# Optimization experiments

Hardware: AMD Instinct MI355X
Metric: run time of the kernel (lower is better)

The kernel has to match this reference:

```python
import jax, jax.numpy as jnp
import numpy as np

H = 16
D_MODEL = 1024
D_K = D_MODEL // H


def setup_inputs() -> dict:
    key = jax.random.key(0)
    ks = jax.random.split(key, 12)
    B, S = 2, 2048
    scale = 1.0 / np.sqrt(D_MODEL)
    inp = {
        "query": jax.random.normal(ks[0], (B, S, D_MODEL), jnp.float32),
        "key": jax.random.normal(ks[1], (B, S, D_MODEL), jnp.float32),
        "value": jax.random.normal(ks[2], (B, S, D_MODEL), jnp.float32),
        "mask": jnp.ones((B, 1, S), jnp.int32),
        "Wq": jax.random.normal(ks[3], (D_MODEL, D_MODEL), jnp.float32) * scale,
        "bq": jnp.zeros((D_MODEL,), jnp.float32),
        "Wk": jax.random.normal(ks[4], (D_MODEL, D_MODEL), jnp.float32) * scale,
        "bk": jnp.zeros((D_MODEL,), jnp.float32),
        "Wv": jax.random.normal(ks[5], (D_MODEL, D_MODEL), jnp.float32) * scale,
        "bv": jnp.zeros((D_MODEL,), jnp.float32),
        "Wo": jax.random.normal(ks[6], (D_MODEL, D_MODEL), jnp.float32) * scale,
        "bo": jnp.zeros((D_MODEL,), jnp.float32),
    }
    return inp


def reference(query, key, value, mask, Wq, bq, Wk, bk, Wv, bv, Wo, bo):
    B, S, _ = query.shape
    # QKV projections, split heads: [B, S, D] -> [B, H, S, d_k]
    def proj(x, W, b):
        y = x @ W.T + b
        return y.reshape(B, -1, H, D_K).transpose(0, 2, 1, 3)

    q = proj(query, Wq, bq)
    k = proj(key, Wk, bk)
    v = proj(value, Wv, bv)

    # scaled dot-product attention with full score matrix [B, H, Sq, Sk]
    scores = jnp.einsum("bhqd,bhkd->bhqk", q, k) / np.sqrt(D_K)
    m = mask[:, None, :, :]  # unsqueeze head dim: [B, 1, 1_or_S, S]
    scores = jnp.where(m == 0, jnp.float32(-1e9), scores)
    p_attn = jax.nn.softmax(scores, axis=-1)  # dropout p=0.0 (eval)
    x = jnp.einsum("bhqk,bhkd->bhqd", p_attn, v)

    # merge heads and output projection
    x = x.transpose(0, 2, 1, 3).reshape(B, -1, H * D_K)
    return x @ Wo.T + bo
```

## Files before the change

kernel.cpp:

```cpp
#include <hip/hip_runtime.h>
#include <hip/hip_bf16.h>
#include <stdint.h>

typedef __bf16 bf8 __attribute__((ext_vector_type(8)));
typedef float  f4  __attribute__((ext_vector_type(4)));

typedef unsigned int __attribute__((address_space(1))) as1_uint;
typedef unsigned int __attribute__((address_space(3))) as3_uint;

__device__ __forceinline__ void async_ld16(const void* g, void* l) {
    __builtin_amdgcn_global_load_lds((as1_uint*)g, (as3_uint*)l, 16, 0, 0);
}

__device__ __forceinline__ unsigned short f2bf(float f) {
    __hip_bfloat16 h = __float2bfloat16(f);
    unsigned short u;
    __builtin_memcpy(&u, &h, 2);
    return u;
}

__global__ __launch_bounds__(256)
void convert_all(const float* __restrict__ s0, const float* __restrict__ s1,
                 const float* __restrict__ s2, const float* __restrict__ s3,
                 const float* __restrict__ s4, const float* __restrict__ s5,
                 const float* __restrict__ s6,
                 unsigned short* __restrict__ d0, unsigned short* __restrict__ d1,
                 unsigned short* __restrict__ d2, unsigned short* __restrict__ d3,
                 unsigned short* __restrict__ d4, unsigned short* __restrict__ d5,
                 unsigned short* __restrict__ d6)
{
    size_t i4 = (((size_t)blockIdx.x * 256) + threadIdx.x) << 2;
    const float* src; unsigned short* dst; size_t off;
    if (i4 < ((size_t)3 << 22)) {
        unsigned seg = (unsigned)(i4 >> 22);
        off = i4 & (((size_t)1 << 22) - 1);
        src = seg == 0 ? s0 : (seg == 1 ? s1 : s2);
        dst = seg == 0 ? d0 : (seg == 1 ? d1 : d2);
    } else {
        size_t j = i4 - ((size_t)3 << 22);
        unsigned seg = (unsigned)(j >> 20);
        off = j & (((size_t)1 << 20) - 1);
        src = seg == 0 ? s3 : (seg == 1 ? s4 : (seg == 2 ? s5 : s6));
        dst = seg == 0 ? d3 : (seg == 1 ? d4 : (seg == 2 ? d5 : d6));
    }
    float4 f = *(const float4*)(src + off);
    ushort4 o;
    o.x = f2bf(f.x); o.y = f2bf(f.y); o.z = f2bf(f.z); o.w = f2bf(f.w);
    *(ushort4*)(dst + off) = o;
}

template<int MODE>
__device__ __forceinline__
void gemm_body(const unsigned short* __restrict__ A,
               const unsigned short* __restrict__ W,
               const float* __restrict__ bias,
               void* __restrict__ out,
               float scale, int bx, int by)
{
    __shared__ unsigned short lA[128 * 32];
    __shared__ unsigned short lB[128 * 32];

    const int tid  = threadIdx.x;
    const int wv   = tid >> 6;
    const int lane = tid & 63;
    const int l15  = lane & 15;
    const int kq   = (lane >> 4) << 3;
    const int srow = lane >> 2;
    const int scol = (lane & 3) << 3;
    const int m0   = by << 7;
    const int n0   = bx << 7;
    const int wm   = (wv >> 1) << 6;
    const int wn   = (wv & 1) << 6;

    f4 acc[4][4];
    const f4 zero = {0.f, 0.f, 0.f, 0.f};
#pragma unroll
    for (int i = 0; i < 4; ++i)
#pragma unroll
        for (int j = 0; j < 4; ++j) acc[i][j] = zero;

    for (int kt = 0; kt < 1024; kt += 32) {
#pragma unroll
        for (int s = 0; s < 2; ++s) {
            const int chunk = wv * 2 + s;
            const int row   = chunk * 16 + srow;
            async_ld16(A + (size_t)(m0 + row) * 1024 + kt + scol, &lA[chunk * 512]);
            async_ld16(W + (size_t)(n0 + row) * 1024 + kt + scol, &lB[chunk * 512]);
        }
        __syncthreads();

        bf8 af[4], bfr[4];
#pragma unroll
        for (int i = 0; i < 4; ++i)
            af[i] = *(const bf8*)&lA[(wm + i * 16 + l15) * 32 + kq];
#pragma unroll
        for (int j = 0; j < 4; ++j)
            bfr[j] = *(const bf8*)&lB[(wn + j * 16 + l15) * 32 + kq];
#pragma unroll
        for (int i = 0; i < 4; ++i)
#pragma unroll
            for (int j = 0; j < 4; ++j)
                acc[i][j] = __builtin_amdgcn_mfma_f32_16x16x32_bf16(af[i], bfr[j], acc[i][j], 0, 0, 0);
        __syncthreads();
    }

    const int cr = (lane >> 4) << 2;
    const int cc = l15;
    if (MODE == 0) {
        unsigned short* o = (unsigned short*)out;
#pragma unroll
        for (int j = 0; j < 4; ++j) {
            const int gn = n0 + wn + j * 16 + cc;
            const float bj = bias[gn];
            const int hh = gn >> 6, dd = gn & 63;
#pragma unroll
            for (int i = 0; i < 4; ++i) {
#pragma unroll
                for (int r = 0; r < 4; ++r) {
                    const int gm = m0 + wm + i * 16 + cr + r;
                    const int bb = gm >> 11, ss = gm & 2047;
                    const float v = (acc[i][j][r] + bj) * scale;
                    o[(((size_t)(bb * 16 + hh) * 2048 + ss) << 6) + dd] = f2bf(v);
                }
            }
        }
    } else {
        float* o = (float*)out;
#pragma unroll
        for (int j = 0; j < 4; ++j) {
            const int gn = n0 + wn + j * 16 + cc;
            const float bj = bias[gn];
#pragma unroll
            for (int i = 0; i < 4; ++i) {
#pragma unroll
                for (int r = 0; r < 4; ++r) {
                    const int gm = m0 + wm + i * 16 + cr + r;
                    o[((size_t)gm << 10) + gn] = acc[i][j][r] + bj;
                }
            }
        }
    }
}

__global__ __launch_bounds__(256)
void gemm_qkv(const unsigned short* __restrict__ XQ, const unsigned short* __restrict__ XK,
              const unsigned short* __restrict__ XV,
              const unsigned short* __restrict__ WQ, const unsigned short* __restrict__ WK,
              const unsigned short* __restrict__ WV,
              const float* __restrict__ bq, const float* __restrict__ bk,
              const float* __restrict__ bv,
              unsigned short* __restrict__ QP, unsigned short* __restrict__ KP,
              unsigned short* __restrict__ VP)
{
    const int z = blockIdx.z;
    const unsigned short* A = z == 0 ? XQ : (z == 1 ? XK : XV);
    const unsigned short* W = z == 0 ? WQ : (z == 1 ? WK : WV);
    const float* b          = z == 0 ? bq : (z == 1 ? bk : bv);
    unsigned short* o       = z == 0 ? QP : (z == 1 ? KP : VP);
    const float scale       = z == 0 ? 0.125f : 1.0f;
    gemm_body<0>(A, W, b, o, scale, blockIdx.x, blockIdx.y);
}

__global__ __launch_bounds__(256)
void gemm_o(const unsigned short* __restrict__ A, const unsigned short* __restrict__ W,
            const float* __restrict__ bias, float* __restrict__ out)
{
    gemm_body<1>(A, W, bias, out, 1.0f, blockIdx.x, blockIdx.y);
}

__global__ __launch_bounds__(256)
void flash_attn(const unsigned short* __restrict__ Qp,
                const unsigned short* __restrict__ Kp,
                const unsigned short* __restrict__ Vp,
                const int* __restrict__ maskp,
                unsigned short* __restrict__ ctx)
{
    __shared__ unsigned short lK[64 * 72];
    __shared__ unsigned short lVt[64 * 64];
    __shared__ float lmask[64];

    const int tid  = threadIdx.x;
    const int wv   = tid >> 6;
    const int lane = tid & 63;
    const int l15  = lane & 15;
    const int quad = lane >> 4;
    const int kq   = quad << 3;
    const int cr   = quad << 2;

    const int q0 = blockIdx.x << 6;
    const int h  = blockIdx.y;
    const int b  = blockIdx.z;

    const size_t headoff = ((size_t)(b * 16 + h)) << 17;
    const unsigned short* Qh = Qp + headoff;
    const unsigned short* Kh = Kp + headoff;
    const unsigned short* Vh = Vp + headoff;

    const unsigned short* qrow = Qh + ((size_t)(q0 + wv * 16 + l15) << 6);
    bf8 qf[2];
    qf[0] = *(const bf8*)(qrow + kq);
    qf[1] = *(const bf8*)(qrow + 32 + kq);

    const f4 zero = {0.f, 0.f, 0.f, 0.f};
    f4 of[4];
#pragma unroll
    for (int mt = 0; mt < 4; ++mt) of[mt] = zero;
    float li = 0.f;

    unsigned short* lPw = &lK[wv * 16 * 72];

    const int srow = tid >> 3;
    const int scol = (tid & 7) << 3;

    for (int kt0 = 0; kt0 < 2048; kt0 += 64) {
        __syncthreads();

#pragma unroll
        for (int it = 0; it < 2; ++it) {
            const int r = srow + it * 32;
            *(uint4*)&lK[r * 72 + scol] = *(const uint4*)(Kh + ((size_t)(kt0 + r) << 6) + scol);
        }
#pragma unroll
        for (int it = 0; it < 2; ++it) {
            const int r = srow + it * 32;
            uint4 dv = *(const uint4*)(Vh + ((size_t)(kt0 + r) << 6) + scol);
            const unsigned short* u = (const unsigned short*)&dv;
            const int rhi = r >> 3, rlo = r & 7;
#pragma unroll
            for (int j = 0; j < 8; ++j) {
                const int d = scol + j;
                lVt[d * 64 + (((rhi + (d >> 3)) & 7) << 3) + rlo] = u[j];
            }
        }
        if (tid < 64)
            lmask[tid] = (maskp[((size_t)b << 11) + kt0 + tid] == 0) ? 0.0f : 1.0f;
        __syncthreads();

        float st[4][4];
#pragma unroll
        for (int t = 0; t < 4; ++t) {
            f4 s = zero;
#pragma unroll
            for (int kb = 0; kb < 2; ++kb) {
                bf8 kf = *(const bf8*)&lK[(t * 16 + l15) * 72 + kb * 32 + kq];
                s = __builtin_amdgcn_mfma_f32_16x16x32_bf16(kf, qf[kb], s, 0, 0, 0);
            }
#pragma unroll
            for (int r = 0; r < 4; ++r) st[t][r] = s[r];
        }
        __syncthreads();

        float rsum = 0.f;
#pragma unroll
        for (int t = 0; t < 4; ++t) {
            const f4 mr = *(const f4*)&lmask[t * 16 + cr];
            unsigned short hp[4];
#pragma unroll
            for (int r = 0; r < 4; ++r) {
                const float p = __expf(st[t][r]) * mr[r];
                rsum += p;
                hp[r] = f2bf(p);
            }
            uint2 w;
            w.x = (unsigned)hp[0] | ((unsigned)hp[1] << 16);
            w.y = (unsigned)hp[2] | ((unsigned)hp[3] << 16);
            *(uint2*)&lPw[l15 * 72 + t * 16 + cr] = w;
        }
        rsum += __shfl_xor(rsum, 16, 64);
        rsum += __shfl_xor(rsum, 32, 64);
        li += rsum;

        bf8 pf0 = *(const bf8*)&lPw[l15 * 72 + kq];
        bf8 pf1 = *(const bf8*)&lPw[l15 * 72 + 32 + kq];

#pragma unroll
        for (int mt = 0; mt < 4; ++mt) {
            const int dd = mt * 16 + l15;
            const int dh = dd >> 3;
            bf8 v0 = *(const bf8*)&lVt[dd * 64 + ((((0 * 4 + quad) + dh) & 7) << 3)];
            of[mt] = __builtin_amdgcn_mfma_f32_16x16x32_bf16(v0, pf0, of[mt], 0, 0, 0);
            bf8 v1 = *(const bf8*)&lVt[dd * 64 + ((((1 * 4 + quad) + dh) & 7) << 3)];
            of[mt] = __builtin_amdgcn_mfma_f32_16x16x32_bf16(v1, pf1, of[mt], 0, 0, 0);
        }
    }

    const float inv = 1.0f / li;
    const int tok = q0 + wv * 16 + l15;
    const size_t rowb = (((size_t)b * 2048 + tok) << 10) + (h << 6);
#pragma unroll
    for (int mt = 0; mt < 4; ++mt) {
        unsigned short hp[4];
#pragma unroll
        for (int r = 0; r < 4; ++r) hp[r] = f2bf(of[mt][r] * inv);
        uint2 w;
        w.x = (unsigned)hp[0] | ((unsigned)hp[1] << 16);
        w.y = (unsigned)hp[2] | ((unsigned)hp[3] << 16);
        *(uint2*)&ctx[rowb + mt * 16 + cr] = w;
    }
}

extern "C" void kernel_launch(void* const* d_in, const int* in_sizes, int n_in,
                              void* d_out, int out_size, void* d_ws, size_t ws_size,
                              hipStream_t stream)
{
    const float* q    = (const float*)d_in[0];
    const float* k    = (const float*)d_in[1];
    const float* v    = (const float*)d_in[2];
    const int*   mask = (const int*)d_in[3];
    const float* Wq   = (const float*)d_in[4];
    const float* bq   = (const float*)d_in[5];
    const float* Wk   = (const float*)d_in[6];
    const float* bk   = (const float*)d_in[7];
    const float* Wv   = (const float*)d_in[8];
    const float* bv   = (const float*)d_in[9];
    const float* Wo   = (const float*)d_in[10];
    const float* bo   = (const float*)d_in[11];
    float* out = (float*)d_out;

    unsigned short* ws  = (unsigned short*)d_ws;
    unsigned short* XQ  = ws;
    unsigned short* XK  = ws + 4194304;
    unsigned short* XV  = ws + 8388608;
    unsigned short* WQb = ws + 12582912;
    unsigned short* WKb = ws + 13631488;
    unsigned short* WVb = ws + 14680064;
    unsigned short* WOb = ws + 15728640;
    unsigned short* QP  = ws + 16777216;
    unsigned short* KP  = ws + 20971520;
    unsigned short* VP  = ws + 25165824;
    unsigned short* CTX = XQ;

    convert_all<<<16384, 256, 0, stream>>>(q, k, v, Wq, Wk, Wv, Wo,
                                           XQ, XK, XV, WQb, WKb, WVb, WOb);
    gemm_qkv<<<dim3(8, 32, 3), 256, 0, stream>>>(XQ, XK, XV, WQb, WKb, WVb,
                                                 bq, bk, bv, QP, KP, VP);
    flash_attn<<<dim3(32, 16, 2), 256, 0, stream>>>(QP, KP, VP, mask, CTX);
    gemm_o<<<dim3(8, 32), 256, 0, stream>>>(CTX, WOb, bo, out);
}
```

Before: 273.4 us.

## Split attention keys across waves, swizzle LDS, narrow output GEMM tiles, vectorize epilogues

The flash attention kernel now has each wave handle 32 queries by 32 keys, with a cross-wave reduction of the output and row sums through shared memory at the end. It also uses XOR-swizzled K and transposed-V layouts in LDS to avoid bank conflicts. The GEMMs swap operand roles so the epilogue can write four contiguous outputs per lane with vector stores and vector bias loads. The output-projection GEMM uses 128x64 tiles on a 16x32 grid to double the block count. The key split and LDS reduction add shared-memory traffic and synchronisation in exchange for more Q reuse per K/V fragment.

```diff
diff --git a/kernel.cpp b/kernel.cpp
--- a/kernel.cpp
+++ b/kernel.cpp
@@ -2,6 +2,7 @@
 #include <hip/hip_bf16.h>
 #include <stdint.h>
 
+typedef unsigned short us;
 typedef __bf16 bf8 __attribute__((ext_vector_type(8)));
 typedef float  f4  __attribute__((ext_vector_type(4)));
 
@@ -12,9 +13,9 @@
     __builtin_amdgcn_global_load_lds((as1_uint*)g, (as3_uint*)l, 16, 0, 0);
 }
 
-__device__ __forceinline__ unsigned short f2bf(float f) {
+__device__ __forceinline__ us f2bf(float f) {
     __hip_bfloat16 h = __float2bfloat16(f);
-    unsigned short u;
+    us u;
     __builtin_memcpy(&u, &h, 2);
     return u;
 }
@@ -24,13 +25,12 @@
                  const float* __restrict__ s2, const float* __restrict__ s3,
                  const float* __restrict__ s4, const float* __restrict__ s5,
                  const float* __restrict__ s6,
-                 unsigned short* __restrict__ d0, unsigned short* __restrict__ d1,
-                 unsigned short* __restrict__ d2, unsigned short* __restrict__ d3,
-                 unsigned short* __restrict__ d4, unsigned short* __restrict__ d5,
-                 unsigned short* __restrict__ d6)
+                 us* __restrict__ d0, us* __restrict__ d1, us* __restrict__ d2,
+                 us* __restrict__ d3, us* __restrict__ d4, us* __restrict__ d5,
+                 us* __restrict__ d6)
 {
     size_t i4 = (((size_t)blockIdx.x * 256) + threadIdx.x) << 2;
-    const float* src; unsigned short* dst; size_t off;
+    const float* src; us* dst; size_t off;
     if (i4 < ((size_t)3 << 22)) {
         unsigned seg = (unsigned)(i4 >> 22);
         off = i4 & (((size_t)1 << 22) - 1);
@@ -49,135 +49,14 @@
     *(ushort4*)(dst + off) = o;
 }
 
-template<int MODE>
+template<int MODE, int BN>
 __device__ __forceinline__
-void gemm_body(const unsigned short* __restrict__ A,
-               const unsigned short* __restrict__ W,
-               const float* __restrict__ bias,
-               void* __restrict__ out,
+void gemm_body(const us* __restrict__ A, const us* __restrict__ W,
+               const float* __restrict__ bias, void* __restrict__ out,
                float scale, int bx, int by)
 {
-    __shared__ unsigned short lA[128 * 32];
-    __shared__ unsigned short lB[128 * 32];
-
-    const int tid  = threadIdx.x;
-    const int wv   = tid >> 6;
-    const int lane = tid & 63;
-    const int l15  = lane & 15;
-    const int kq   = (lane >> 4) << 3;
-    const int srow = lane >> 2;
-    const int scol = (lane & 3) << 3;
-    const int m0   = by << 7;
-    const int n0   = bx << 7;
-    const int wm   = (wv >> 1) << 6;
-    const int wn   = (wv & 1) << 6;
-
-    f4 acc[4][4];
-    const f4 zero = {0.f, 0.f, 0.f, 0.f};
-#pragma unroll
-    for (int i = 0; i < 4; ++i)
-#pragma unroll
-        for (int j = 0; j < 4; ++j) acc[i][j] = zero;
-
-    for (int kt = 0; kt < 1024; kt += 32) {
-#pragma unroll
-        for (int s = 0; s < 2; ++s) {
-            const int chunk = wv * 2 + s;
-            const int row   = chunk * 16 + srow;
-            async_ld16(A + (size_t)(m0 + row) * 1024 + kt + scol, &lA[chunk * 512]);
-            async_ld16(W + (size_t)(n0 + row) * 1024 + kt + scol, &lB[chunk * 512]);
-        }
-        __syncthreads();
-
-        bf8 af[4], bfr[4];
-#pragma unroll
-        for (int i = 0; i < 4; ++i)
-            af[i] = *(const bf8*)&lA[(wm + i * 16 + l15) * 32 + kq];
-#pragma unroll
-        for (int j = 0; j < 4; ++j)
-            bfr[j] = *(const bf8*)&lB[(wn + j * 16 + l15) * 32 + kq];
-#pragma unroll
-        for (int i = 0; i < 4; ++i)
-#pragma unroll
-            for (int j = 0; j < 4; ++j)
-                acc[i][j] = __builtin_amdgcn_mfma_f32_16x16x32_bf16(af[i], bfr[j], acc[i][j], 0, 0, 0);
-        __syncthreads();
-    }
-
-    const int cr = (lane >> 4) << 2;
-    const int cc = l15;
-    if (MODE == 0) {
-        unsigned short* o = (unsigned short*)out;
-#pragma unroll
-        for (int j = 0; j < 4; ++j) {
-            const int gn = n0 + wn + j * 16 + cc;
-            const float bj = bias[gn];
-            const int hh = gn >> 6, dd = gn & 63;
-#pragma unroll
-            for (int i = 0; i < 4; ++i) {
-#pragma unroll
-                for (int r = 0; r < 4; ++r) {
-                    const int gm = m0 + wm + i * 16 + cr + r;
-                    const int bb = gm >> 11, ss = gm & 2047;
-                    const float v = (acc[i][j][r] + bj) * scale;
-                    o[(((size_t)(bb * 16 + hh) * 2048 + ss) << 6) + dd] = f2bf(v);
-                }
-            }
-        }
-    } else {
-        float* o = (float*)out;
-#pragma unroll
-        for (int j = 0; j < 4; ++j) {
-            const int gn = n0 + wn + j * 16 + cc;
-            const float bj = bias[gn];
-#pragma unroll
-            for (int i = 0; i < 4; ++i) {
-#pragma unroll
-                for (int r = 0; r < 4; ++r) {
-                    const int gm = m0 + wm + i * 16 + cr + r;
-                    o[((size_t)gm << 10) + gn] = acc[i][j][r] + bj;
-                }
-            }
-        }
-    }
-}
-
-__global__ __launch_bounds__(256)
-void gemm_qkv(const unsigned short* __restrict__ XQ, const unsigned short* __restrict__ XK,
-              const unsigned short* __restrict__ XV,
-              const unsigned short* __restrict__ WQ, const unsigned short* __restrict__ WK,
-              const unsigned short* __restrict__ WV,
-              const float* __restrict__ bq, const float* __restrict__ bk,
-              const float* __restrict__ bv,
-              unsigned short* __restrict__ QP, unsigned short* __restrict__ KP,
-              unsigned short* __restrict__ VP)
-{
-    const int z = blockIdx.z;
-    const unsigned short* A = z == 0 ? XQ : (z == 1 ? XK : XV);
-    const unsigned short* W = z == 0 ? WQ : (z == 1 ? WK : WV);
-    const float* b          = z == 0 ? bq : (z == 1 ? bk : bv);
-    unsigned short* o       = z == 0 ? QP : (z == 1 ? KP : VP);
-    const float scale       = z == 0 ? 0.125f : 1.0f;
-    gemm_body<0>(A, W, b, o, scale, blockIdx.x, blockIdx.y);
-}
-
-__global__ __launch_bounds__(256)
-void gemm_o(const unsigned short* __restrict__ A, const unsigned short* __restrict__ W,
-            const float* __restrict__ bias, float* __restrict__ out)
-{
-    gemm_body<1>(A, W, bias, out, 1.0f, blockIdx.x, blockIdx.y);
-}
-
-__global__ __launch_bounds__(256)
-void flash_attn(const unsigned short* __restrict__ Qp,
-                const unsigned short* __restrict__ Kp,
-                const unsigned short* __restrict__ Vp,
-                const int* __restrict__ maskp,
-                unsigned short* __restrict__ ctx)
-{
-    __shared__ unsigned short lK[64 * 72];
-    __shared__ unsigned short lVt[64 * 64];
-    __shared__ float lmask[64];
+    __shared__ us lA[128 * 32];
+    __shared__ us lB[BN * 32];
 
     const int tid  = threadIdx.x;
     const int wv   = tid >> 6;
@@ -186,116 +65,294 @@
     const int quad = lane >> 4;
     const int kq   = quad << 3;
     const int cr   = quad << 2;
+    const int srow = lane >> 2;
+    const int scol = (lane & 3) << 3;
+    const int m0   = by << 7;
+    const int n0   = bx * BN;
+    constexpr int MJ = (BN == 128) ? 4 : 2;
+    const int wm = (BN == 128) ? ((wv >> 1) << 6) : (wv << 5);
+    const int wn = (BN == 128) ? ((wv & 1) << 6) : 0;
+
+    f4 acc[4][MJ];
+    const f4 zero = {0.f, 0.f, 0.f, 0.f};
+#pragma unroll
+    for (int i = 0; i < 4; ++i)
+#pragma unroll
+        for (int j = 0; j < MJ; ++j) acc[i][j] = zero;
+
+    for (int kt = 0; kt < 1024; kt += 32) {
+#pragma unroll
+        for (int s = 0; s < 2; ++s) {
+            const int chunk = wv * 2 + s;
+            const int row   = chunk * 16 + srow;
+            async_ld16(A + (size_t)(m0 + row) * 1024 + kt + scol, &lA[chunk * 512]);
+        }
+        if (BN == 128) {
+#pragma unroll
+            for (int s = 0; s < 2; ++s) {
+                const int chunk = wv * 2 + s;
+                const int row   = chunk * 16 + srow;
+                async_ld16(W + (size_t)(n0 + row) * 1024 + kt + scol, &lB[chunk * 512]);
+            }
+        } else {
+            const int row = wv * 16 + srow;
+            async_ld16(W + (size_t)(n0 + row) * 1024 + kt + scol, &lB[wv * 512]);
+        }
+        __syncthreads();
+
+        bf8 wf[4], xf[MJ];
+#pragma unroll
+        for (int i = 0; i < 4; ++i)
+            wf[i] = *(const bf8*)&lB[(wn + i * 16 + l15) * 32 + kq];
+#pragma unroll
+        for (int j = 0; j < MJ; ++j)
+            xf[j] = *(const bf8*)&lA[(wm + j * 16 + l15) * 32 + kq];
+#pragma unroll
+        for (int i = 0; i < 4; ++i)
+#pragma unroll
+            for (int j = 0; j < MJ; ++j)
+                acc[i][j] = __builtin_amdgcn_mfma_f32_16x16x32_bf16(wf[i], xf[j], acc[i][j], 0, 0, 0);
+        __syncthreads();
+    }
+
+#pragma unroll
+    for (int i = 0; i < 4; ++i) {
+        const int gnb = n0 + wn + i * 16 + cr;
+        const f4 bj = *(const f4*)&bias[gnb];
+        if (MODE == 0) {
+            us* o = (us*)out;
+            const int hh = gnb >> 6, dd = gnb & 63;
+#pragma unroll
+            for (int j = 0; j < MJ; ++j) {
+                const int gm = m0 + wm + j * 16 + l15;
+                const int bb = gm >> 11, ss = gm & 2047;
+                us hp[4];
+#pragma unroll
+                for (int r = 0; r < 4; ++r)
+                    hp[r] = f2bf((acc[i][j][r] + bj[r]) * scale);
+                uint2 w;
+                w.x = (unsigned)hp[0] | ((unsigned)hp[1] << 16);
+                w.y = (unsigned)hp[2] | ((unsigned)hp[3] << 16);
+                *(uint2*)&o[(((size_t)(bb * 16 + hh) * 2048 + ss) << 6) + dd] = w;
+            }
+        } else {
+            float* o = (float*)out;
+#pragma unroll
+            for (int j = 0; j < MJ; ++j) {
+                const int gm = m0 + wm + j * 16 + l15;
+                f4 v;
+#pragma unroll
+                for (int r = 0; r < 4; ++r) v[r] = acc[i][j][r] + bj[r];
+                *(f4*)&o[((size_t)gm << 10) + gnb] = v;
+            }
+        }
+    }
+}
+
+__global__ __launch_bounds__(256)
+void gemm_qkv(const us* __restrict__ XQ, const us* __restrict__ XK,
+              const us* __restrict__ XV,
+              const us* __restrict__ WQ, const us* __restrict__ WK,
+              const us* __restrict__ WV,
+              const float* __restrict__ bq, const float* __restrict__ bk,
+              const float* __restrict__ bv,
+              us* __restrict__ QP, us* __restrict__ KP, us* __restrict__ VP)
+{
+    const int z = blockIdx.z;
+    const us* A = z == 0 ? XQ : (z == 1 ? XK : XV);
+    const us* W = z == 0 ? WQ : (z == 1 ? WK : WV);
+    const float* b = z == 0 ? bq : (z == 1 ? bk : bv);
+    us* o = z == 0 ? QP : (z == 1 ? KP : VP);
+    const float scale = z == 0 ? 0.125f : 1.0f;
+    gemm_body<0, 128>(A, W, b, o, scale, blockIdx.x, blockIdx.y);
+}
+
+__global__ __launch_bounds__(256)
+void gemm_o(const us* __restrict__ A, const us* __restrict__ W,
+            const float* __restrict__ bias, float* __restrict__ out)
+{
+    gemm_body<1, 64>(A, W, bias, out, 1.0f, blockIdx.x, blockIdx.y);
+}
+
+__global__ __launch_bounds__(256)
+void flash_attn(const us* __restrict__ Qp, const us* __restrict__ Kp,
+                const us* __restrict__ Vp, const int* __restrict__ maskp,
+                us* __restrict__ ctx)
+{
+    __shared__ char smem[27136];
+    us* lK    = (us*)smem;
+    us* lVt   = (us*)(smem + 8192);
+    us* lP    = (us*)(smem + 16384);
+    float* lmask = (float*)(smem + 26624);
+    float* liRed = (float*)(smem + 26880);
+    float* red   = (float*)smem;
+
+    const int tid  = threadIdx.x;
+    const int wv   = tid >> 6;
+    const int lane = tid & 63;
+    const int l15  = lane & 15;
+    const int quad = lane >> 4;
+    const int cr   = quad << 2;
+    const int qh   = wv & 1;
+    const int kh   = wv >> 1;
 
     const int q0 = blockIdx.x << 6;
     const int h  = blockIdx.y;
     const int b  = blockIdx.z;
 
     const size_t headoff = ((size_t)(b * 16 + h)) << 17;
-    const unsigned short* Qh = Qp + headoff;
-    const unsigned short* Kh = Kp + headoff;
-    const unsigned short* Vh = Vp + headoff;
-
-    const unsigned short* qrow = Qh + ((size_t)(q0 + wv * 16 + l15) << 6);
-    bf8 qf[2];
-    qf[0] = *(const bf8*)(qrow + kq);
-    qf[1] = *(const bf8*)(qrow + 32 + kq);
+    const us* Qh = Qp + headoff;
+    const us* Kh = Kp + headoff;
+    const us* Vh = Vp + headoff;
+
+    bf8 qf[2][2];
+#pragma unroll
+    for (int nt = 0; nt < 2; ++nt)
+#pragma unroll
+        for (int kb = 0; kb < 2; ++kb)
+            qf[nt][kb] = *(const bf8*)(Qh + ((size_t)(q0 + qh * 32 + nt * 16 + l15) << 6)
+                                          + kb * 32 + (quad << 3));
 
     const f4 zero = {0.f, 0.f, 0.f, 0.f};
-    f4 of[4];
-#pragma unroll
-    for (int mt = 0; mt < 4; ++mt) of[mt] = zero;
-    float li = 0.f;
-
-    unsigned short* lPw = &lK[wv * 16 * 72];
-
-    const int srow = tid >> 3;
-    const int scol = (tid & 7) << 3;
+    f4 of[4][2];
+#pragma unroll
+    for (int mt = 0; mt < 4; ++mt)
+#pragma unroll
+        for (int nt = 0; nt < 2; ++nt) of[mt][nt] = zero;
+    float li[2] = {0.f, 0.f};
+
+    us* lPw = lP + wv * (32 * 40);
+    const int sc = tid & 7;
+    const int sr = tid >> 3;
+    const int ls = lane >> 3;
 
     for (int kt0 = 0; kt0 < 2048; kt0 += 64) {
         __syncthreads();
 
 #pragma unroll
         for (int it = 0; it < 2; ++it) {
-            const int r = srow + it * 32;
-            *(uint4*)&lK[r * 72 + scol] = *(const uint4*)(Kh + ((size_t)(kt0 + r) << 6) + scol);
+            const int r = sr + 32 * it;
+            uint4 kv = *(const uint4*)(Kh + ((size_t)(kt0 + r) << 6) + sc * 8);
+            *(uint4*)&lK[r * 64 + ((sc ^ ls) << 3)] = kv;
         }
 #pragma unroll
         for (int it = 0; it < 2; ++it) {
-            const int r = srow + it * 32;
-            uint4 dv = *(const uint4*)(Vh + ((size_t)(kt0 + r) << 6) + scol);
-            const unsigned short* u = (const unsigned short*)&dv;
-            const int rhi = r >> 3, rlo = r & 7;
-#pragma unroll
-            for (int j = 0; j < 8; ++j) {
-                const int d = scol + j;
-                lVt[d * 64 + (((rhi + (d >> 3)) & 7) << 3) + rlo] = u[j];
+            const int r = sr + 32 * it;
+            uint4 vv = *(const uint4*)(Vh + ((size_t)(kt0 + r) << 6) + sc * 8);
+            const us* u = (const us*)&vv;
+            const int rhi = r >> 3;
+#pragma unroll
+            for (int jj = 0; jj < 8; ++jj) {
+                const int d = sc * 8 + jj;
+                const int p = (rhi ^ jj ^ sc) & 7;
+                lVt[d * 64 + (p << 3) + ls] = u[jj];
             }
         }
         if (tid < 64)
             lmask[tid] = (maskp[((size_t)b << 11) + kt0 + tid] == 0) ? 0.0f : 1.0f;
         __syncthreads();
 
-        float st[4][4];
-#pragma unroll
-        for (int t = 0; t < 4; ++t) {
-            f4 s = zero;
+        f4 st[2][2];
+#pragma unroll
+        for (int mt2 = 0; mt2 < 2; ++mt2)
+#pragma unroll
+            for (int nt = 0; nt < 2; ++nt) st[mt2][nt] = zero;
+#pragma unroll
+        for (int mt2 = 0; mt2 < 2; ++mt2) {
+            const int key = kh * 32 + mt2 * 16 + l15;
 #pragma unroll
             for (int kb = 0; kb < 2; ++kb) {
-                bf8 kf = *(const bf8*)&lK[(t * 16 + l15) * 72 + kb * 32 + kq];
-                s = __builtin_amdgcn_mfma_f32_16x16x32_bf16(kf, qf[kb], s, 0, 0, 0);
-            }
-#pragma unroll
-            for (int r = 0; r < 4; ++r) st[t][r] = s[r];
-        }
-        __syncthreads();
-
-        float rsum = 0.f;
-#pragma unroll
-        for (int t = 0; t < 4; ++t) {
-            const f4 mr = *(const f4*)&lmask[t * 16 + cr];
-            unsigned short hp[4];
-#pragma unroll
-            for (int r = 0; r < 4; ++r) {
-                const float p = __expf(st[t][r]) * mr[r];
-                rsum += p;
-                hp[r] = f2bf(p);
-            }
-            uint2 w;
-            w.x = (unsigned)hp[0] | ((unsigned)hp[1] << 16);
-            w.y = (unsigned)hp[2] | ((unsigned)hp[3] << 16);
-            *(uint2*)&lPw[l15 * 72 + t * 16 + cr] = w;
-        }
-        rsum += __shfl_xor(rsum, 16, 64);
-        rsum += __shfl_xor(rsum, 32, 64);
-        li += rsum;
-
-        bf8 pf0 = *(const bf8*)&lPw[l15 * 72 + kq];
-        bf8 pf1 = *(const bf8*)&lPw[l15 * 72 + 32 + kq];
-
+                const int c = 4 * kb + quad;
+                bf8 kf = *(const bf8*)&lK[key * 64 + ((c ^ (l15 & 7)) << 3)];
+#pragma unroll
+                for (int nt = 0; nt < 2; ++nt)
+                    st[mt2][nt] = __builtin_amdgcn_mfma_f32_16x16x32_bf16(kf, qf[nt][kb], st[mt2][nt], 0, 0, 0);
+            }
+        }
+
+        float rs[2] = {0.f, 0.f};
+#pragma unroll
+        for (int mt2 = 0; mt2 < 2; ++mt2) {
+            const f4 mr = *(const f4*)&lmask[kh * 32 + mt2 * 16 + cr];
+#pragma unroll
+            for (int nt = 0; nt < 2; ++nt) {
+                us hp[4];
+#pragma unroll
+                for (int r = 0; r < 4; ++r) {
+                    const float pv = __expf(st[mt2][nt][r]) * mr[r];
+                    rs[nt] += pv;
+                    hp[r] = f2bf(pv);
+                }
+                uint2 w;
+                w.x = (unsigned)hp[0] | ((unsigned)hp[1] << 16);
+                w.y = (unsigned)hp[2] | ((unsigned)hp[3] << 16);
+                *(uint2*)&lPw[(nt * 16 + l15) * 40 + mt2 * 16 + cr] = w;
+            }
+        }
+#pragma unroll
+        for (int nt = 0; nt < 2; ++nt) {
+            float r2 = rs[nt];
+            r2 += __shfl_xor(r2, 16, 64);
+            r2 += __shfl_xor(r2, 32, 64);
+            li[nt] += r2;
+        }
+
+        bf8 pf[2];
+#pragma unroll
+        for (int nt = 0; nt < 2; ++nt)
+            pf[nt] = *(const bf8*)&lPw[(nt * 16 + l15) * 40 + (quad << 3)];
 #pragma unroll
         for (int mt = 0; mt < 4; ++mt) {
             const int dd = mt * 16 + l15;
-            const int dh = dd >> 3;
-            bf8 v0 = *(const bf8*)&lVt[dd * 64 + ((((0 * 4 + quad) + dh) & 7) << 3)];
-            of[mt] = __builtin_amdgcn_mfma_f32_16x16x32_bf16(v0, pf0, of[mt], 0, 0, 0);
-            bf8 v1 = *(const bf8*)&lVt[dd * 64 + ((((1 * 4 + quad) + dh) & 7) << 3)];
-            of[mt] = __builtin_amdgcn_mfma_f32_16x16x32_bf16(v1, pf1, of[mt], 0, 0, 0);
-        }
-    }
-
-    const float inv = 1.0f / li;
-    const int tok = q0 + wv * 16 + l15;
-    const size_t rowb = (((size_t)b * 2048 + tok) << 10) + (h << 6);
-#pragma unroll
-    for (int mt = 0; mt < 4; ++mt) {
-        unsigned short hp[4];
-#pragma unroll
-        for (int r = 0; r < 4; ++r) hp[r] = f2bf(of[mt][r] * inv);
-        uint2 w;
-        w.x = (unsigned)hp[0] | ((unsigned)hp[1] << 16);
-        w.y = (unsigned)hp[2] | ((unsigned)hp[3] << 16);
-        *(uint2*)&ctx[rowb + mt * 16 + cr] = w;
+            const int c  = 4 * kh + quad;
+            const int p  = (c ^ (dd & 7) ^ ((dd >> 3) & 7)) & 7;
+            bf8 vf = *(const bf8*)&lVt[dd * 64 + (p << 3)];
+#pragma unroll
+            for (int nt = 0; nt < 2; ++nt)
+                of[mt][nt] = __builtin_amdgcn_mfma_f32_16x16x32_bf16(vf, pf[nt], of[mt][nt], 0, 0, 0);
+        }
+    }
+
+    __syncthreads();
+    if (kh == 1) {
+#pragma unroll
+        for (int mt = 0; mt < 4; ++mt)
+#pragma unroll
+            for (int nt = 0; nt < 2; ++nt)
+#pragma unroll
+                for (int r = 0; r < 4; ++r)
+                    red[qh * 2048 + (mt * 16 + cr + r) * 32 + nt * 16 + l15] = of[mt][nt][r];
+        if (quad == 0) {
+#pragma unroll
+            for (int nt = 0; nt < 2; ++nt)
+                liRed[qh * 32 + nt * 16 + l15] = li[nt];
+        }
+    }
+    __syncthreads();
+    if (kh == 0) {
+#pragma unroll
+        for (int mt = 0; mt < 4; ++mt)
+#pragma unroll
+            for (int nt = 0; nt < 2; ++nt)
+#pragma unroll
+                for (int r = 0; r < 4; ++r)
+                    of[mt][nt][r] += red[qh * 2048 + (mt * 16 + cr + r) * 32 + nt * 16 + l15];
+#pragma unroll
+        for (int nt = 0; nt < 2; ++nt) {
+            const float linv = 1.0f / (li[nt] + liRed[qh * 32 + nt * 16 + l15]);
+            const int tok = q0 + qh * 32 + nt * 16 + l15;
+            const size_t rowb = (((size_t)b * 2048 + tok) << 10) + (h << 6);
+#pragma unroll
+            for (int mt = 0; mt < 4; ++mt) {
+                us hp[4];
+#pragma unroll
+                for (int r = 0; r < 4; ++r) hp[r] = f2bf(of[mt][nt][r] * linv);
+                uint2 w;
+                w.x = (unsigned)hp[0] | ((unsigned)hp[1] << 16);
+                w.y = (unsigned)hp[2] | ((unsigned)hp[3] << 16);
+                *(uint2*)&ctx[rowb + mt * 16 + cr] = w;
+            }
+        }
     }
 }
 
@@ -317,23 +374,23 @@
     const float* bo   = (const float*)d_in[11];
     float* out = (float*)d_out;
 
-    unsigned short* ws  = (unsigned short*)d_ws;
-    unsigned short* XQ  = ws;
-    unsigned short* XK  = ws + 4194304;
-    unsigned short* XV  = ws + 8388608;
-    unsigned short* WQb = ws + 12582912;
-    unsigned short* WKb = ws + 13631488;
-    unsigned short* WVb = ws + 14680064;
-    unsigned short* WOb = ws + 15728640;
-    unsigned short* QP  = ws + 16777216;
-    unsigned short* KP  = ws + 20971520;
-    unsigned short* VP  = ws + 25165824;
-    unsigned short* CTX = XQ;
+    us* ws  = (us*)d_ws;
+    us* XQ  = ws;
+    us* XK  = ws + 4194304;
+    us* XV  = ws + 8388608;
+    us* WQb = ws + 12582912;
+    us* WKb = ws + 13631488;
+    us* WVb = ws + 14680064;
+    us* WOb = ws + 15728640;
+    us* QP  = ws + 16777216;
+    us* KP  = ws + 20971520;
+    us* VP  = ws + 25165824;
+    us* CTX = XQ;
 
     convert_all<<<16384, 256, 0, stream>>>(q, k, v, Wq, Wk, Wv, Wo,
                                            XQ, XK, XV, WQb, WKb, WVb, WOb);
     gemm_qkv<<<dim3(8, 32, 3), 256, 0, stream>>>(XQ, XK, XV, WQb, WKb, WVb,
                                                  bq, bk, bv, QP, KP, VP);
     flash_attn<<<dim3(32, 16, 2), 256, 0, stream>>>(QP, KP, VP, mask, CTX);
-    gemm_o<<<dim3(8, 32), 256, 0, stream>>>(CTX, WOb, bo, out);
-}
+    gemm_o<<<dim3(16, 32), 256, 0, stream>>>(CTX, WOb, bo, out);
+}
```

New measurement: 272.2 us. About the same (-0.5%).
